# Kernel tuning notes

Hardware: AMD Instinct MI355X
Metric: run time of the kernel (lower is better)

The kernel has to match this reference:

```python
import jax, jax.numpy as jnp
import numpy as np

HIDDEN = 4096
N_HEADS = 32
N_KV_HEADS = 8
HEAD_DIM = 128
ROPE_THETA = 10000.0


def setup_inputs() -> dict:
    key = jax.random.key(0)
    ks = jax.random.split(key, 5)
    B, S = 1, 2048
    scale = 0.02
    return {
        "hidden_states": jax.random.normal(ks[0], (B, S, HIDDEN), dtype=jnp.float32),
        "q_w": jax.random.normal(ks[1], (N_HEADS * HEAD_DIM, HIDDEN), dtype=jnp.float32) * scale,
        "k_w": jax.random.normal(ks[2], (N_KV_HEADS * HEAD_DIM, HIDDEN), dtype=jnp.float32) * scale,
        "v_w": jax.random.normal(ks[3], (N_KV_HEADS * HEAD_DIM, HIDDEN), dtype=jnp.float32) * scale,
        "o_w": jax.random.normal(ks[4], (HIDDEN, N_HEADS * HEAD_DIM), dtype=jnp.float32) * scale,
        "position_ids": jnp.arange(S, dtype=jnp.int64 if jax.config.jax_enable_x64 else jnp.int32)[None, :],
    }


def _rotate_half(x):
    h = x.shape[-1] // 2
    return jnp.concatenate((-x[..., h:], x[..., :h]), axis=-1)


def _rope_cos_sin(position_ids, dtype):
    # default rope: inv_freq = theta^(-arange(0,hd,2)/hd), attention_scaling = 1
    inv_freq = 1.0 / (ROPE_THETA ** (jnp.arange(0, HEAD_DIM, 2, dtype=jnp.float32) / HEAD_DIM))
    freqs = position_ids.astype(jnp.float32)[:, :, None] * inv_freq[None, None, :]  # [B,S,hd/2]
    emb = jnp.concatenate((freqs, freqs), axis=-1)  # [B,S,hd]
    return jnp.cos(emb).astype(dtype), jnp.sin(emb).astype(dtype)


def reference(hidden_states, q_w, k_w, v_w, o_w, position_ids):
    B, S, _ = hidden_states.shape
    n_rep = N_HEADS // N_KV_HEADS

    q = (hidden_states @ q_w.T).reshape(B, S, N_HEADS, HEAD_DIM).transpose(0, 2, 1, 3)
    k = (hidden_states @ k_w.T).reshape(B, S, N_KV_HEADS, HEAD_DIM).transpose(0, 2, 1, 3)
    v = (hidden_states @ v_w.T).reshape(B, S, N_KV_HEADS, HEAD_DIM).transpose(0, 2, 1, 3)

    cos, sin = _rope_cos_sin(position_ids, hidden_states.dtype)
    cos = cos[:, None, :, :]  # unsqueeze head dim
    sin = sin[:, None, :, :]
    q = q * cos + _rotate_half(q) * sin
    k = k * cos + _rotate_half(k) * sin

    # repeat_kv (GQA)
    k = jnp.repeat(k, n_rep, axis=1)  # [B,H,S,hd]
    v = jnp.repeat(v, n_rep, axis=1)

    scale = HEAD_DIM ** -0.5
    scores = jnp.einsum("bhqd,bhkd->bhqk", q, k) * scale  # [B,H,S,S]
    causal = jnp.tril(jnp.ones((S, S), dtype=bool))
    scores = jnp.where(causal[None, None, :, :], scores, jnp.finfo(scores.dtype).min)
    probs = jax.nn.softmax(scores, axis=-1)
    attn = jnp.einsum("bhqk,bhkd->bhqd", probs, v)  # [B,H,S,hd]

    attn = attn.transpose(0, 2, 1, 3).reshape(B, S, N_HEADS * HEAD_DIM)
    return attn @ o_w.T
```

## Files before the change

kernel.cpp:

```cpp
#include <hip/hip_runtime.h>
#include <hip/hip_bf16.h>

#define NH   32
#define NKV  8
#define HD   128
#define SL   2048
#define HID  4096
#define KVW  1024
#define QKVN 6144

typedef __attribute__((ext_vector_type(8))) short short8;
typedef __attribute__((ext_vector_type(4))) float f32x4;

static __device__ __forceinline__ unsigned short f2bf(float f){
  union { float f; unsigned int i; } v; v.f = f;
  unsigned int r = v.i + 0x7FFFu + ((v.i >> 16) & 1u);
  return (unsigned short)(r >> 16);
}
static __device__ __forceinline__ float bf2f(unsigned short u){
  union { unsigned int i; float f; } v; v.i = ((unsigned int)u) << 16; return v.f;
}
static __device__ __forceinline__ unsigned int pack2(float lo, float hi){
  return (unsigned int)f2bf(lo) | ((unsigned int)f2bf(hi) << 16);
}
static __device__ __forceinline__ unsigned int cvtpk(float lo, float hi){
  unsigned int d;
  asm("v_cvt_pk_bf16_f32 %0, %1, %2" : "=v"(d) : "v"(lo), "v"(hi));
  return d;
}

static __device__ __forceinline__ void gload_lds16(const void* g, void* l){
  __builtin_amdgcn_global_load_lds(
      (const __attribute__((address_space(1))) void*)g,
      (__attribute__((address_space(3))) void*)l,
      16, 0, 0);
}

__global__ void cast_f32_bf16(const float* __restrict__ src, uint4* __restrict__ dst, int n8){
  int stride = gridDim.x * blockDim.x;
  for (int i = blockIdx.x * blockDim.x + threadIdx.x; i < n8; i += stride){
    float4 a = ((const float4*)src)[2*i + 0];
    float4 b = ((const float4*)src)[2*i + 1];
    uint4 o;
    o.x = pack2(a.x, a.y); o.y = pack2(a.z, a.w);
    o.z = pack2(b.x, b.y); o.w = pack2(b.z, b.w);
    dst[i] = o;
  }
}

__global__ void rope_table_kernel(const int* __restrict__ pos, float2* __restrict__ tab){
  int i = blockIdx.x * blockDim.x + threadIdx.x;
  if (i >= SL * 64) return;
  int s = i >> 6, f = i & 63;
  float inv = expf(-((float)(2 * f) / 128.0f) * 9.210340371976184f);
  float ang = (float)pos[s] * inv;
  float sn, cs;
  sincosf(ang, &sn, &cs);
  tab[i] = make_float2(cs, sn);
}

__global__ void rope_apply_kernel(unsigned short* x, const float2* __restrict__ tab,
                                  int nheads, int rowstride){
  int i = blockIdx.x * blockDim.x + threadIdx.x;
  int total = SL * nheads * 64;
  if (i >= total) return;
  int f = i & 63;
  int t = i >> 6;
  int h = t % nheads;
  int s = t / nheads;
  float2 cs = tab[s * 64 + f];
  size_t base = (size_t)s * rowstride + h * HD;
  float x1 = bf2f(x[base + f]);
  float x2 = bf2f(x[base + f + 64]);
  x[base + f]      = f2bf(x1 * cs.x - x2 * cs.y);
  x[base + f + 64] = f2bf(x2 * cs.x + x1 * cs.y);
}

template<bool F32OUT>
__global__ __launch_bounds__(256) void gemm_bt(
  const unsigned short* __restrict__ A,
  const unsigned short* __restrict__ B,
  void* __restrict__ Cp, int M, int N, int K)
{
  __shared__ __align__(16) unsigned short As[2][128 * 32];
  __shared__ __align__(16) unsigned short Bs[2][128 * 32];
  const int tid = threadIdx.x;
  const int lane = tid & 63, wid = tid >> 6;
  const int g = lane >> 4, c15 = lane & 15;
  const int wr = wid >> 1, wc = wid & 1;

  const int gx = gridDim.x, gy = gridDim.y;
  const int nwg = gx * gy;
  const int lin = blockIdx.y * gx + blockIdx.x;
  int mb, nb;
  const int cpx = nwg >> 3;
  const int RN  = cpx >> 3;
  if (RN > 0 && (gy & 7) == 0 && (cpx & 7) == 0 && gx % RN == 0 && (8 % (gx / RN)) == 0){
    int xcd = lin & 7, j = lin >> 3;
    int nrc = gx / RN;
    int rr = xcd / nrc, rc = xcd % nrc;
    mb = rr * 8 + (j & 7);
    nb = rc * RN + (j >> 3);
  } else {
    mb = lin / gx; nb = lin % gx;
  }
  const int m0 = mb * 128, n0 = nb * 128;

  const int srow = wid * 32 + (lane >> 2);
  const int scol = (lane & 3) * 8;
  const unsigned short* Ag = &A[(size_t)(m0 + srow) * K + scol];
  const unsigned short* Bg = &B[(size_t)(n0 + srow) * K + scol];
  const size_t K16 = (size_t)16 * K;

  f32x4 acc[4][4] = {};

  gload_lds16(Ag,       &As[0][wid * 1024]);
  gload_lds16(Ag + K16, &As[0][wid * 1024 + 512]);
  gload_lds16(Bg,       &Bs[0][wid * 1024]);
  gload_lds16(Bg + K16, &Bs[0][wid * 1024 + 512]);
  __syncthreads();

  const int nk = K >> 5;
  for (int t = 0; t < nk; ++t){
    const int cur = t & 1;
    if (t + 1 < nk){
      const unsigned short* a2 = Ag + (size_t)(t + 1) * 32;
      const unsigned short* b2 = Bg + (size_t)(t + 1) * 32;
      const int nb2 = cur ^ 1;
      gload_lds16(a2,       &As[nb2][wid * 1024]);
      gload_lds16(a2 + K16, &As[nb2][wid * 1024 + 512]);
      gload_lds16(b2,       &Bs[nb2][wid * 1024]);
      gload_lds16(b2 + K16, &Bs[nb2][wid * 1024 + 512]);
    }
    short8 af[4], bfr[4];
#pragma unroll
    for (int m = 0; m < 4; ++m)
      af[m] = *(const short8*)(&As[cur][(wr * 64 + m * 16 + c15) * 32 + g * 8]);
#pragma unroll
    for (int n = 0; n < 4; ++n)
      bfr[n] = *(const short8*)(&Bs[cur][(wc * 64 + n * 16 + c15) * 32 + g * 8]);
#pragma unroll
    for (int m = 0; m < 4; ++m)
#pragma unroll
      for (int n = 0; n < 4; ++n)
        acc[m][n] = __builtin_amdgcn_mfma_f32_16x16x32_bf16(af[m], bfr[n], acc[m][n], 0, 0, 0);
    __syncthreads();
  }

#pragma unroll
  for (int m = 0; m < 4; ++m)
#pragma unroll
    for (int n = 0; n < 4; ++n){
      int row = m0 + wr * 64 + m * 16 + g * 4;
      int col = n0 + wc * 64 + n * 16 + c15;
      f32x4 v = acc[m][n];
      if (F32OUT){
        float* C = (float*)Cp;
#pragma unroll
        for (int r = 0; r < 4; ++r) C[(size_t)(row + r) * N + col] = v[r];
      } else {
        unsigned short* C = (unsigned short*)Cp;
#pragma unroll
        for (int r = 0; r < 4; ++r) C[(size_t)(row + r) * N + col] = f2bf(v[r]);
      }
    }
}

__global__ void transpose_v_kernel(const unsigned short* __restrict__ v, int vstride,
                                   unsigned short* __restrict__ vt){
  __shared__ unsigned short t[64][65];
  int h  = blockIdx.z;
  int d0 = blockIdx.y * 64;
  int s0 = blockIdx.x * 64;
  int c  = threadIdx.x & 63;
  int r0 = threadIdx.x >> 6;
#pragma unroll
  for (int r = r0; r < 64; r += 4) t[r][c] = v[(size_t)(s0 + r) * vstride + h * HD + d0 + c];
  __syncthreads();
#pragma unroll
  for (int r = r0; r < 64; r += 4) vt[(size_t)(h * HD + d0 + r) * SL + s0 + c] = t[c][r];
}

__global__ __launch_bounds__(512, 4) void flash_attn_kernel(
  const unsigned short* __restrict__ Q,
  const unsigned short* __restrict__ Kb,
  const unsigned short* __restrict__ Vt,
  unsigned short* __restrict__ O)
{
  __shared__ __align__(16) unsigned short Ks[64 * 128];
  __shared__ __align__(16) unsigned short Vs[128 * 64];
  const int tid = threadIdx.x, lane = tid & 63, wid = tid >> 6;
  const int g = lane >> 4, c15 = lane & 15;
  const int kvh = blockIdx.x;
  const int yy = blockIdx.y;
  const int qb = (yy & 1) ? (yy >> 1) : (63 - (yy >> 1));
  const int h = kvh * 4 + (wid & 3);
  const int rg = wid >> 2;
  const int q0 = qb * 32;
  const int qg = q0 + rg * 16 + c15;

  short8 aq[4];
  {
    size_t qrow = (size_t)qg * QKVN + h * HD;
#pragma unroll
    for (int kk = 0; kk < 4; ++kk)
      aq[kk] = *(const short8*)(&Q[qrow + kk * 32 + g * 8]);
  }

  const int krow = tid >> 3, kcol = (tid & 7) * 8;
  const int vrow = tid >> 2, vcol = (tid & 3) * 8;
  const unsigned short* Kgb = Kb + (size_t)kvh * HD;
  const unsigned short* Vgb = Vt + ((size_t)kvh * HD + vrow) * SL;

  uint4 kr0, kr1, vr0, vr1;
  {
    const unsigned short* kg = Kgb + (size_t)krow * QKVN + kcol;
    kr0 = *(const uint4*)kg; kr1 = *(const uint4*)(kg + 64);
    const unsigned short* vg = Vgb + vcol;
    vr0 = *(const uint4*)vg; vr1 = *(const uint4*)(vg + 32);
  }

  float m_i = -1e30f, l_i = 0.f;
  f32x4 oacc[8];
#pragma unroll
  for (int df = 0; df < 8; ++df) oacc[df] = (f32x4){0.f, 0.f, 0.f, 0.f};

  const float scl2 = 0.08838834764831845f * 1.4426950408889634f;
  const int nt = (q0 + 31) / 64 + 1;
  for (int kt = 0; kt < nt; ++kt){
    *(uint4*)((char*)Ks + krow * 256 + (( kcol * 2       ) ^ ((krow & 7) << 4))) = kr0;
    *(uint4*)((char*)Ks + krow * 256 + (((kcol * 2) + 128) ^ ((krow & 7) << 4))) = kr1;
    *(uint4*)((char*)Vs + vrow * 128 + (( vcol * 2       ) ^ ((vrow & 7) << 4))) = vr0;
    *(uint4*)((char*)Vs + vrow * 128 + (((vcol * 2) +  64) ^ ((vrow & 7) << 4))) = vr1;
    __syncthreads();

    if (kt + 1 < nt){
      const unsigned short* kg = Kgb + (size_t)((kt + 1) * 64 + krow) * QKVN + kcol;
      kr0 = *(const uint4*)kg; kr1 = *(const uint4*)(kg + 64);
      const unsigned short* vg = Vgb + (kt + 1) * 64 + vcol;
      vr0 = *(const uint4*)vg; vr1 = *(const uint4*)(vg + 32);
    }

    f32x4 sc[4];
    __builtin_amdgcn_s_setprio(1);
#pragma unroll
    for (int f = 0; f < 4; ++f){
      sc[f] = (f32x4){0.f, 0.f, 0.f, 0.f};
#pragma unroll
      for (int kk = 0; kk < 4; ++kk){
        short8 bk = *(const short8*)((const char*)Ks + (f * 16 + c15) * 256 +
                                     ((kk * 64 + g * 16) ^ ((c15 & 7) << 4)));
        sc[f] = __builtin_amdgcn_mfma_f32_16x16x32_bf16(bk, aq[kk], sc[f], 0, 0, 0);
      }
    }
    __builtin_amdgcn_s_setprio(0);

    float p[4][4];
#pragma unroll
    for (int f = 0; f < 4; ++f)
#pragma unroll
      for (int r = 0; r < 4; ++r){
        int kvg = kt * 64 + f * 16 + g * 4 + r;
        p[f][r] = (kvg <= qg) ? sc[f][r] * scl2 : -1e30f;
      }

    float pmax = p[0][0];
#pragma unroll
    for (int f = 0; f < 4; ++f)
#pragma unroll
      for (int r = 0; r < 4; ++r) pmax = fmaxf(pmax, p[f][r]);
    pmax = fmaxf(pmax, __shfl_xor(pmax, 16, 64));
    pmax = fmaxf(pmax, __shfl_xor(pmax, 32, 64));

    if (!__all(pmax - m_i <= 8.0f)){
      float mnew = fmaxf(m_i, pmax);
      float cf = exp2f(m_i - mnew);
      float cfr[4];
#pragma unroll
      for (int r = 0; r < 4; ++r) cfr[r] = __shfl(cf, (lane & 48) | (g * 4 + r), 64);
#pragma unroll
      for (int df = 0; df < 8; ++df)
#pragma unroll
        for (int r = 0; r < 4; ++r) oacc[df][r] *= cfr[r];
      l_i *= cf;
      m_i = mnew;
    }

    float lsum = 0.f;
#pragma unroll
    for (int f = 0; f < 4; ++f)
#pragma unroll
      for (int r = 0; r < 4; ++r){ float e = exp2f(p[f][r] - m_i); p[f][r] = e; lsum += e; }
    lsum += __shfl_xor(lsum, 16, 64);
    lsum += __shfl_xor(lsum, 32, 64);
    l_i += lsum;

    unsigned int pd[4][2];
#pragma unroll
    for (int f = 0; f < 4; ++f){
      pd[f][0] = cvtpk(p[f][0], p[f][1]);
      pd[f][1] = cvtpk(p[f][2], p[f][3]);
    }

    const int src0 = ((g & 1) << 5) | c15;
    const int src1 = src0 + 16;
    const bool hiF = (g >= 2);
#pragma unroll
    for (int kk = 0; kk < 2; ++kk){
      union { unsigned int u[4]; short8 s8; } pa;
#pragma unroll
      for (int pr = 0; pr < 2; ++pr){
        unsigned int a0 = __shfl((int)pd[2 * kk + 0][pr], src0, 64);
        unsigned int b0 = __shfl((int)pd[2 * kk + 1][pr], src0, 64);
        unsigned int a1 = __shfl((int)pd[2 * kk + 0][pr], src1, 64);
        unsigned int b1 = __shfl((int)pd[2 * kk + 1][pr], src1, 64);
        pa.u[pr]     = hiF ? b0 : a0;
        pa.u[2 + pr] = hiF ? b1 : a1;
      }
      __builtin_amdgcn_s_setprio(1);
#pragma unroll
      for (int df = 0; df < 8; ++df){
        short8 bv = *(const short8*)((const char*)Vs + (df * 16 + c15) * 128 +
                                     ((kk * 64 + g * 16) ^ ((c15 & 7) << 4)));
        oacc[df] = __builtin_amdgcn_mfma_f32_16x16x32_bf16(pa.s8, bv, oacc[df], 0, 0, 0);
      }
      __builtin_amdgcn_s_setprio(0);
    }
    __syncthreads();
  }

  float lr[4];
#pragma unroll
  for (int r = 0; r < 4; ++r) lr[r] = __shfl(l_i, (lane & 48) | (g * 4 + r), 64);
#pragma unroll
  for (int df = 0; df < 8; ++df)
#pragma unroll
    for (int r = 0; r < 4; ++r){
      int row = q0 + rg * 16 + g * 4 + r;
      O[(size_t)row * HID + h * HD + df * 16 + c15] = f2bf(oacc[df][r] / lr[r]);
    }
}

extern "C" void kernel_launch(void* const* d_in, const int* in_sizes, int n_in,
                              void* d_out, int out_size, void* d_ws, size_t ws_size,
                              hipStream_t stream)
{
  const float* hs  = (const float*)d_in[0];
  const float* qw  = (const float*)d_in[1];
  const float* kw  = (const float*)d_in[2];
  const float* vw  = (const float*)d_in[3];
  const float* ow  = (const float*)d_in[4];
  const int*   pos = (const int*)d_in[5];

  char* w = (char*)d_ws;
  auto alloc = [&](size_t bytes){ char* p = w; w += (bytes + 255) & ~(size_t)255; return p; };
  unsigned short* xb   = (unsigned short*)alloc((size_t)SL * HID * 2);
  unsigned short* wqkv = (unsigned short*)alloc((size_t)QKVN * HID * 2);
  unsigned short* owb  = (unsigned short*)alloc((size_t)HID * HID * 2);
  unsigned short* qkv  = (unsigned short*)alloc((size_t)SL * QKVN * 2);
  unsigned short* vt   = (unsigned short*)alloc((size_t)SL * KVW * 2);
  unsigned short* ab   = (unsigned short*)alloc((size_t)SL * HID * 2);
  float2*         tab  = (float2*)alloc((size_t)SL * 64 * sizeof(float2));

  auto cast = [&](const float* s, unsigned short* d, long n){
    int n8 = (int)(n / 8);
    int blocks = (n8 + 255) / 256; if (blocks > 2048) blocks = 2048;
    cast_f32_bf16<<<blocks, 256, 0, stream>>>(s, (uint4*)d, n8);
  };
  cast(hs, xb, (long)SL * HID);
  cast(qw, wqkv,                              (long)HID * HID);
  cast(kw, wqkv + (size_t)HID * HID,          (long)KVW * HID);
  cast(vw, wqkv + (size_t)(HID + KVW) * HID,  (long)KVW * HID);
  cast(ow, owb,                               (long)HID * HID);

  rope_table_kernel<<<(SL * 64 + 255) / 256, 256, 0, stream>>>(pos, tab);

  gemm_bt<false><<<dim3(QKVN / 128, SL / 128), 256, 0, stream>>>(xb, wqkv, qkv, SL, QKVN, HID);

  rope_apply_kernel<<<(SL * NH  * 64 + 255) / 256, 256, 0, stream>>>(qkv,        tab, NH,  QKVN);
  rope_apply_kernel<<<(SL * NKV * 64 + 255) / 256, 256, 0, stream>>>(qkv + HID,  tab, NKV, QKVN);

  transpose_v_kernel<<<dim3(SL / 64, HD / 64, NKV), 256, 0, stream>>>(qkv + HID + KVW, QKVN, vt);

  flash_attn_kernel<<<dim3(NKV, SL / 32), 512, 0, stream>>>(qkv, qkv + HID, vt, ab);

  gemm_bt<true><<<dim3(HID / 128, SL / 128), 256, 0, stream>>>(ab, owb, d_out, SL, HID, HID);
}
```

Measured before the change: 366.5 us.

## Replace GEMM with 8-wave larger-tile kernel using swizzled LDS and staged prefetch

Replaces the 128x128 4-wave GEMM with an 8-wave kernel that uses 256x256 tiles for the QKV projection and 128x256 for the output projection, with a K step of 64. Shared memory is XOR-swizzled to avoid bank conflicts, and next-tile global-to-LDS loads are split across compute phases with explicit vmcnt waits, raw barriers and setprio around the MFMA blocks. The aim is more data reuse per tile and better overlap of loads with matrix math. In exchange it uses more LDS and registers, and the QKV grid becomes small (24x8 blocks), which may underfill the CUs.

```diff
diff --git a/kernel.cpp b/kernel.cpp
--- a/kernel.cpp
+++ b/kernel.cpp
@@ -76,18 +76,20 @@
   x[base + f + 64] = f2bf(x2 * cs.x + x1 * cs.y);
 }
 
-template<bool F32OUT>
-__global__ __launch_bounds__(256) void gemm_bt(
+template<int BM, bool F32OUT>
+__global__ __launch_bounds__(512, 2) void gemm_bt8(
   const unsigned short* __restrict__ A,
   const unsigned short* __restrict__ B,
   void* __restrict__ Cp, int M, int N, int K)
 {
-  __shared__ __align__(16) unsigned short As[2][128 * 32];
-  __shared__ __align__(16) unsigned short Bs[2][128 * 32];
+  constexpr int BN = 256;
+  constexpr int MF = BM / 32;
+  __shared__ __align__(16) unsigned short As[2 * BM * 64];
+  __shared__ __align__(16) unsigned short Bs[2 * BN * 64];
   const int tid = threadIdx.x;
   const int lane = tid & 63, wid = tid >> 6;
   const int g = lane >> 4, c15 = lane & 15;
-  const int wr = wid >> 1, wc = wid & 1;
+  const int wr = wid >> 2, wn = wid & 3;
 
   const int gx = gridDim.x, gy = gridDim.y;
   const int nwg = gx * gy;
@@ -101,58 +103,127 @@
     int rr = xcd / nrc, rc = xcd % nrc;
     mb = rr * 8 + (j & 7);
     nb = rc * RN + (j >> 3);
-  } else {
-    mb = lin / gx; nb = lin % gx;
+  } else { mb = lin / gx; nb = lin % gx; }
+  const int m0 = mb * BM, n0 = nb * BN;
+
+  const int lr = lane >> 3;
+  const int ls = (lane & 7) ^ lr;
+  const unsigned short* Agl = A + (size_t)(m0 + wid * (BM / 8) + lr) * K + ls * 8;
+  const unsigned short* Bgl = B + (size_t)(n0 + wid * 32 + lr) * K + ls * 8;
+  unsigned short* AsW = As + wid * (BM / 8) * 64;
+  unsigned short* BsW = Bs + wid * 32 * 64;
+
+  auto STA = [&](int b, int q, int tt){
+    gload_lds16(Agl + (size_t)q * 8 * K + tt * 64, AsW + b * BM * 64 + q * 512);
+  };
+  auto STB = [&](int b, int q, int tt){
+    gload_lds16(Bgl + (size_t)q * 8 * K + tt * 64, BsW + b * BN * 64 + q * 512);
+  };
+  auto ldA = [&](int b, int fm, int kk) -> short8 {
+    return *(const short8*)((const char*)As + (size_t)b * BM * 128 +
+           (wr * (BM / 2) + fm * 16 + c15) * 128 +
+           ((kk * 64 + g * 16) ^ ((c15 & 7) << 4)));
+  };
+  auto ldB = [&](int b, int fn, int kk) -> short8 {
+    return *(const short8*)((const char*)Bs + (size_t)b * BN * 128 +
+           (wn * 64 + fn * 16 + c15) * 128 +
+           ((kk * 64 + g * 16) ^ ((c15 & 7) << 4)));
+  };
+
+  f32x4 acc[MF][4] = {};
+
+#pragma unroll
+  for (int q = 0; q < BM / 64; ++q) STA(0, q, 0);
+#pragma unroll
+  for (int q = 0; q < 4; ++q) STB(0, q, 0);
+
+  const int nk = K >> 6;
+  for (int t = 0; t < nk; ++t){
+    const int cur = t & 1, nxt = cur ^ 1;
+    const bool pf = (t + 1 < nk);
+    const int t1 = t + 1;
+    short8 af[4], bf[4];
+
+    if (pf){
+      STA(nxt, 0, t1); STA(nxt, 1, t1);
+      if constexpr (BM == 128){
+        STB(nxt, 0, t1);
+        asm volatile("s_waitcnt vmcnt(3)" ::: "memory");
+      } else {
+        asm volatile("s_waitcnt vmcnt(2)" ::: "memory");
+      }
+    } else {
+      asm volatile("s_waitcnt vmcnt(0)" ::: "memory");
+    }
+    __builtin_amdgcn_s_barrier();
+#pragma unroll
+    for (int m = 0; m < 4; ++m) af[m] = ldA(cur, m, 0);
+#pragma unroll
+    for (int n = 0; n < 4; ++n) bf[n] = ldB(cur, n, 0);
+    __builtin_amdgcn_s_setprio(1);
+#pragma unroll
+    for (int m = 0; m < 4; ++m)
+#pragma unroll
+      for (int n = 0; n < 4; ++n)
+        acc[m][n] = __builtin_amdgcn_mfma_f32_16x16x32_bf16(af[m], bf[n], acc[m][n], 0, 0, 0);
+    __builtin_amdgcn_s_setprio(0);
+    __builtin_amdgcn_s_barrier();
+
+    if constexpr (BM == 256){
+#pragma unroll
+      for (int m = 0; m < 4; ++m) af[m] = ldA(cur, 4 + m, 0);
+      if (pf){ STA(nxt, 2, t1); STA(nxt, 3, t1); }
+      __builtin_amdgcn_s_barrier();
+      __builtin_amdgcn_s_setprio(1);
+#pragma unroll
+      for (int m = 0; m < 4; ++m)
+#pragma unroll
+        for (int n = 0; n < 4; ++n)
+          acc[4 + m][n] = __builtin_amdgcn_mfma_f32_16x16x32_bf16(af[m], bf[n], acc[4 + m][n], 0, 0, 0);
+      __builtin_amdgcn_s_setprio(0);
+      __builtin_amdgcn_s_barrier();
+    }
+
+#pragma unroll
+    for (int m = 0; m < 4; ++m) af[m] = ldA(cur, m, 1);
+#pragma unroll
+    for (int n = 0; n < 4; ++n) bf[n] = ldB(cur, n, 1);
+    if (pf){
+      if constexpr (BM == 256){ STB(nxt, 0, t1); STB(nxt, 1, t1); }
+      else                    { STB(nxt, 1, t1); STB(nxt, 2, t1); STB(nxt, 3, t1); }
+    }
+    __builtin_amdgcn_s_barrier();
+    __builtin_amdgcn_s_setprio(1);
+#pragma unroll
+    for (int m = 0; m < 4; ++m)
+#pragma unroll
+      for (int n = 0; n < 4; ++n)
+        acc[m][n] = __builtin_amdgcn_mfma_f32_16x16x32_bf16(af[m], bf[n], acc[m][n], 0, 0, 0);
+    __builtin_amdgcn_s_setprio(0);
+    __builtin_amdgcn_s_barrier();
+
+    if constexpr (BM == 256){
+#pragma unroll
+      for (int m = 0; m < 4; ++m) af[m] = ldA(cur, 4 + m, 1);
+      if (pf){ STB(nxt, 2, t1); STB(nxt, 3, t1); }
+      __builtin_amdgcn_s_barrier();
+      __builtin_amdgcn_s_setprio(1);
+#pragma unroll
+      for (int m = 0; m < 4; ++m)
+#pragma unroll
+        for (int n = 0; n < 4; ++n)
+          acc[4 + m][n] = __builtin_amdgcn_mfma_f32_16x16x32_bf16(af[m], bf[n], acc[4 + m][n], 0, 0, 0);
+      __builtin_amdgcn_s_setprio(0);
+      __builtin_amdgcn_s_barrier();
+    }
   }
-  const int m0 = mb * 128, n0 = nb * 128;
-
-  const int srow = wid * 32 + (lane >> 2);
-  const int scol = (lane & 3) * 8;
-  const unsigned short* Ag = &A[(size_t)(m0 + srow) * K + scol];
-  const unsigned short* Bg = &B[(size_t)(n0 + srow) * K + scol];
-  const size_t K16 = (size_t)16 * K;
-
-  f32x4 acc[4][4] = {};
-
-  gload_lds16(Ag,       &As[0][wid * 1024]);
-  gload_lds16(Ag + K16, &As[0][wid * 1024 + 512]);
-  gload_lds16(Bg,       &Bs[0][wid * 1024]);
-  gload_lds16(Bg + K16, &Bs[0][wid * 1024 + 512]);
-  __syncthreads();
-
-  const int nk = K >> 5;
-  for (int t = 0; t < nk; ++t){
-    const int cur = t & 1;
-    if (t + 1 < nk){
-      const unsigned short* a2 = Ag + (size_t)(t + 1) * 32;
-      const unsigned short* b2 = Bg + (size_t)(t + 1) * 32;
-      const int nb2 = cur ^ 1;
-      gload_lds16(a2,       &As[nb2][wid * 1024]);
-      gload_lds16(a2 + K16, &As[nb2][wid * 1024 + 512]);
-      gload_lds16(b2,       &Bs[nb2][wid * 1024]);
-      gload_lds16(b2 + K16, &Bs[nb2][wid * 1024 + 512]);
-    }
-    short8 af[4], bfr[4];
-#pragma unroll
-    for (int m = 0; m < 4; ++m)
-      af[m] = *(const short8*)(&As[cur][(wr * 64 + m * 16 + c15) * 32 + g * 8]);
-#pragma unroll
-    for (int n = 0; n < 4; ++n)
-      bfr[n] = *(const short8*)(&Bs[cur][(wc * 64 + n * 16 + c15) * 32 + g * 8]);
-#pragma unroll
-    for (int m = 0; m < 4; ++m)
-#pragma unroll
-      for (int n = 0; n < 4; ++n)
-        acc[m][n] = __builtin_amdgcn_mfma_f32_16x16x32_bf16(af[m], bfr[n], acc[m][n], 0, 0, 0);
-    __syncthreads();
-  }
-
-#pragma unroll
-  for (int m = 0; m < 4; ++m)
+
+#pragma unroll
+  for (int m = 0; m < MF; ++m)
 #pragma unroll
     for (int n = 0; n < 4; ++n){
-      int row = m0 + wr * 64 + m * 16 + g * 4;
-      int col = n0 + wc * 64 + n * 16 + c15;
+      int row = m0 + wr * (BM / 2) + m * 16 + g * 4;
+      int col = n0 + wn * 64 + n * 16 + c15;
       f32x4 v = acc[m][n];
       if (F32OUT){
         float* C = (float*)Cp;
@@ -375,7 +446,7 @@
 
   rope_table_kernel<<<(SL * 64 + 255) / 256, 256, 0, stream>>>(pos, tab);
 
-  gemm_bt<false><<<dim3(QKVN / 128, SL / 128), 256, 0, stream>>>(xb, wqkv, qkv, SL, QKVN, HID);
+  gemm_bt8<256, false><<<dim3(QKVN / 256, SL / 256), 512, 0, stream>>>(xb, wqkv, qkv, SL, QKVN, HID);
 
   rope_apply_kernel<<<(SL * NH  * 64 + 255) / 256, 256, 0, stream>>>(qkv,        tab, NH,  QKVN);
   rope_apply_kernel<<<(SL * NKV * 64 + 255) / 256, 256, 0, stream>>>(qkv + HID,  tab, NKV, QKVN);
@@ -384,5 +455,5 @@
 
   flash_attn_kernel<<<dim3(NKV, SL / 32), 512, 0, stream>>>(qkv, qkv + HID, vt, ab);
 
-  gemm_bt<true><<<dim3(HID / 128, SL / 128), 256, 0, stream>>>(ab, owb, d_out, SL, HID, HID);
-}
+  gemm_bt8<128, true><<<dim3(HID / 256, SL / 128), 512, 0, stream>>>(ab, owb, d_out, SL, HID, HID);
+}
```

Result: slower. 384.0 us (+4.8%).

## Add 256x256 four-phase pipelined GEMM kernel for QKV projection

Applied to the files above, without the earlier changes.

Replaces the 128x128 tiled QKV projection GEMM with a new 512-thread kernel that computes 256x256 output tiles with BK=64. The K loop is split into four phases that interleave LDS fragment reads, staged global-to-LDS prefetches two steps ahead, and MFMA bursts under raised wave priority. LDS reads use an XOR swizzle to avoid bank conflicts. The goal is more data reuse per tile and better overlap of memory with compute, at the cost of more LDS and registers and only 96 workgroups for this problem shape.

```diff
diff --git a/kernel.cpp b/kernel.cpp
--- a/kernel.cpp
+++ b/kernel.cpp
@@ -76,6 +76,158 @@
   x[base + f + 64] = f2bf(x2 * cs.x + x1 * cs.y);
 }
 
+__global__ __launch_bounds__(512, 2) void gemm_qkv4p(
+  const unsigned short* __restrict__ A,
+  const unsigned short* __restrict__ B,
+  unsigned short* __restrict__ C,
+  int M, int N, int K)
+{
+  __shared__ __align__(16) unsigned short As[2][256 * 64];
+  __shared__ __align__(16) unsigned short Bs[2][256 * 64];
+  const int tid = threadIdx.x;
+  const int lane = tid & 63, wid = tid >> 6;
+  const int g = lane >> 4, c15 = lane & 15;
+  const int wr = wid >> 2, wn = wid & 3;
+
+  const int gx = gridDim.x, gy = gridDim.y;
+  const int nwg = gx * gy;
+  const int lin = blockIdx.y * gx + blockIdx.x;
+  int mb, nb;
+  const int cpx = nwg >> 3;
+  const int RN  = cpx >> 3;
+  if (RN > 0 && (gy & 7) == 0 && (cpx & 7) == 0 && gx % RN == 0 && (8 % (gx / RN)) == 0){
+    int xcd = lin & 7, j = lin >> 3;
+    int nrc = gx / RN;
+    int rr = xcd / nrc, rc = xcd % nrc;
+    mb = rr * 8 + (j & 7);
+    nb = rc * RN + (j >> 3);
+  } else { mb = lin / gx; nb = lin % gx; }
+  const int m0 = mb * 256, n0 = nb * 256;
+
+  const int lr8 = lane >> 3;
+  const int gsl = (lane & 7) ^ lr8;
+  const unsigned short* Ag = A + (size_t)(m0 + lr8) * K + gsl * 8;
+  const unsigned short* Bg = B + (size_t)(n0 + lr8) * K + gsl * 8;
+  auto STA = [&](int b, int R, int t){ gload_lds16(Ag + (size_t)R * K + t * 64, &As[b][R * 64]); };
+  auto STB = [&](int b, int R, int t){ gload_lds16(Bg + (size_t)R * K + t * 64, &Bs[b][R * 64]); };
+  const int aR0a = wid * 8,        aR0b = 128 + wid * 8;
+  const int aR1a = 64 + wid * 8,   aR1b = 192 + wid * 8;
+  const int bR0a = 64 * (wid >> 1) + 16 * (wid & 1), bR0b = bR0a + 8;
+  const int bR1a = bR0a + 32,      bR1b = bR0b + 32;
+
+  auto ldA = [&](int b, int row, int kk) -> short8 {
+    return *(const short8*)((const char*)&As[b][0] + row * 128 +
+                            ((kk * 64 + g * 16) ^ ((c15 & 7) << 4)));
+  };
+  auto ldB = [&](int b, int row, int kk) -> short8 {
+    return *(const short8*)((const char*)&Bs[b][0] + row * 128 +
+                            ((kk * 64 + g * 16) ^ ((c15 & 7) << 4)));
+  };
+
+  f32x4 acc[8][4] = {};
+
+  STA(0, aR0a, 0); STA(0, aR0b, 0); STA(0, aR1a, 0); STA(0, aR1b, 0);
+  STB(0, bR0a, 0); STB(0, bR0b, 0); STB(0, bR1a, 0); STB(0, bR1b, 0);
+  STA(1, aR0a, 1); STA(1, aR0b, 1);
+  STB(1, bR0a, 1); STB(1, bR0b, 1);
+  STA(1, aR1a, 1); STA(1, aR1b, 1);
+  asm volatile("s_waitcnt vmcnt(6)" ::: "memory");
+  __builtin_amdgcn_s_barrier();
+
+  const int nk = K >> 6;
+  short8 af[8], b0f[4], b1f[4];
+  for (int t = 0; t < nk; ++t){
+    const int cur = t & 1, nxt = cur ^ 1;
+    const bool pf1 = (t + 1 < nk), pf2 = (t + 2 < nk);
+    const int t1 = t + 1, t2 = t + 2;
+
+#pragma unroll
+    for (int m = 0; m < 4; ++m){
+      int row = wr * 128 + m * 16 + c15;
+      af[m * 2 + 0] = ldA(cur, row, 0); af[m * 2 + 1] = ldA(cur, row, 1);
+    }
+#pragma unroll
+    for (int n = 0; n < 2; ++n){
+      int row = wn * 64 + n * 16 + c15;
+      b0f[n * 2 + 0] = ldB(cur, row, 0); b0f[n * 2 + 1] = ldB(cur, row, 1);
+    }
+    if (pf1){ STB(nxt, bR1a, t1); STB(nxt, bR1b, t1); }
+    __builtin_amdgcn_s_barrier();
+    __builtin_amdgcn_s_setprio(1);
+#pragma unroll
+    for (int m = 0; m < 4; ++m)
+#pragma unroll
+      for (int n = 0; n < 2; ++n){
+        acc[m][n] = __builtin_amdgcn_mfma_f32_16x16x32_bf16(af[m*2+0], b0f[n*2+0], acc[m][n], 0, 0, 0);
+        acc[m][n] = __builtin_amdgcn_mfma_f32_16x16x32_bf16(af[m*2+1], b0f[n*2+1], acc[m][n], 0, 0, 0);
+      }
+    __builtin_amdgcn_s_setprio(0);
+    __builtin_amdgcn_s_barrier();
+
+#pragma unroll
+    for (int n = 0; n < 2; ++n){
+      int row = wn * 64 + 32 + n * 16 + c15;
+      b1f[n * 2 + 0] = ldB(cur, row, 0); b1f[n * 2 + 1] = ldB(cur, row, 1);
+    }
+    if (pf2){ STA(cur, aR0a, t2); STA(cur, aR0b, t2); }
+    __builtin_amdgcn_s_barrier();
+    __builtin_amdgcn_s_setprio(1);
+#pragma unroll
+    for (int m = 0; m < 4; ++m)
+#pragma unroll
+      for (int n = 0; n < 2; ++n){
+        acc[m][2+n] = __builtin_amdgcn_mfma_f32_16x16x32_bf16(af[m*2+0], b1f[n*2+0], acc[m][2+n], 0, 0, 0);
+        acc[m][2+n] = __builtin_amdgcn_mfma_f32_16x16x32_bf16(af[m*2+1], b1f[n*2+1], acc[m][2+n], 0, 0, 0);
+      }
+    __builtin_amdgcn_s_setprio(0);
+    __builtin_amdgcn_s_barrier();
+
+#pragma unroll
+    for (int m = 0; m < 4; ++m){
+      int row = wr * 128 + 64 + m * 16 + c15;
+      af[m * 2 + 0] = ldA(cur, row, 0); af[m * 2 + 1] = ldA(cur, row, 1);
+    }
+    if (pf2){ STB(cur, bR0a, t2); STB(cur, bR0b, t2); }
+    __builtin_amdgcn_s_barrier();
+    __builtin_amdgcn_s_setprio(1);
+#pragma unroll
+    for (int m = 0; m < 4; ++m)
+#pragma unroll
+      for (int n = 0; n < 2; ++n){
+        acc[4+m][n] = __builtin_amdgcn_mfma_f32_16x16x32_bf16(af[m*2+0], b0f[n*2+0], acc[4+m][n], 0, 0, 0);
+        acc[4+m][n] = __builtin_amdgcn_mfma_f32_16x16x32_bf16(af[m*2+1], b0f[n*2+1], acc[4+m][n], 0, 0, 0);
+      }
+    __builtin_amdgcn_s_setprio(0);
+    __builtin_amdgcn_s_barrier();
+
+    if (pf2){ STA(cur, aR1a, t2); STA(cur, aR1b, t2); }
+    __builtin_amdgcn_s_barrier();
+    __builtin_amdgcn_s_setprio(1);
+#pragma unroll
+    for (int m = 0; m < 4; ++m)
+#pragma unroll
+      for (int n = 0; n < 2; ++n){
+        acc[4+m][2+n] = __builtin_amdgcn_mfma_f32_16x16x32_bf16(af[m*2+0], b1f[n*2+0], acc[4+m][2+n], 0, 0, 0);
+        acc[4+m][2+n] = __builtin_amdgcn_mfma_f32_16x16x32_bf16(af[m*2+1], b1f[n*2+1], acc[4+m][2+n], 0, 0, 0);
+      }
+    __builtin_amdgcn_s_setprio(0);
+    if (pf2)      asm volatile("s_waitcnt vmcnt(6)" ::: "memory");
+    else if (pf1) asm volatile("s_waitcnt vmcnt(0)" ::: "memory");
+    __builtin_amdgcn_s_barrier();
+  }
+
+#pragma unroll
+  for (int fm = 0; fm < 8; ++fm)
+#pragma unroll
+    for (int fn = 0; fn < 4; ++fn){
+      int row = m0 + wr * 128 + fm * 16 + g * 4;
+      int col = n0 + wn * 64 + fn * 16 + c15;
+      f32x4 v = acc[fm][fn];
+#pragma unroll
+      for (int r = 0; r < 4; ++r) C[(size_t)(row + r) * N + col] = f2bf(v[r]);
+    }
+}
+
 template<bool F32OUT>
 __global__ __launch_bounds__(256) void gemm_bt(
   const unsigned short* __restrict__ A,
@@ -101,9 +253,7 @@
     int rr = xcd / nrc, rc = xcd % nrc;
     mb = rr * 8 + (j & 7);
     nb = rc * RN + (j >> 3);
-  } else {
-    mb = lin / gx; nb = lin % gx;
-  }
+  } else { mb = lin / gx; nb = lin % gx; }
   const int m0 = mb * 128, n0 = nb * 128;
 
   const int srow = wid * 32 + (lane >> 2);
@@ -375,7 +525,7 @@
 
   rope_table_kernel<<<(SL * 64 + 255) / 256, 256, 0, stream>>>(pos, tab);
 
-  gemm_bt<false><<<dim3(QKVN / 128, SL / 128), 256, 0, stream>>>(xb, wqkv, qkv, SL, QKVN, HID);
+  gemm_qkv4p<<<dim3(QKVN / 256, SL / 256), 512, 0, stream>>>(xb, wqkv, qkv, SL, QKVN, HID);
 
   rope_apply_kernel<<<(SL * NH  * 64 + 255) / 256, 256, 0, stream>>>(qkv,        tab, NH,  QKVN);
   rope_apply_kernel<<<(SL * NKV * 64 + 255) / 256, 256, 0, stream>>>(qkv + HID,  tab, NKV, QKVN);
```

Measured after the change: 371.7 us. Within noise of the previous version (+1.4%).
